# Performance work log

Hardware: AMD Instinct MI355X
Metric: run time of the kernel (lower is better)

The kernel has to match this reference:

```python
import jax, jax.numpy as jnp
import numpy as np

C = 128
K = 5
M = 150000   # num vertices
NF = 300000  # num faces
D = 192      # volume side
NEG_SLOPE = 0.2


def _x_shift(K):
    # Exactly replicates the torch module's grid construction.
    grid = np.linspace(-K // 2, K // 2, K)
    grid_3d = np.stack(np.meshgrid(grid, grid, grid), axis=0).transpose(2, 1, 3, 0)
    return jnp.asarray(grid_3d.reshape(-1, 3), jnp.float32)  # [K^3, 3]


def _trilinear_border(vol, g):
    # vol: [D1, D2, D3]; g: [N, 3] normalized coords in (x, y, z) order
    # (x -> D3/W, y -> D2/H, z -> D1/D), align_corners=True, padding_mode='border'.
    D1, D2, D3 = vol.shape
    def pix(c, S):
        return jnp.clip((c + 1.0) * 0.5 * (S - 1), 0.0, S - 1.0)
    ix, iy, iz = pix(g[:, 0], D3), pix(g[:, 1], D2), pix(g[:, 2], D1)
    x0f, y0f, z0f = jnp.floor(ix), jnp.floor(iy), jnp.floor(iz)
    wx, wy, wz = ix - x0f, iy - y0f, iz - z0f
    x0 = x0f.astype(jnp.int32); y0 = y0f.astype(jnp.int32); z0 = z0f.astype(jnp.int32)
    x1 = jnp.minimum(x0 + 1, D3 - 1)
    y1 = jnp.minimum(y0 + 1, D2 - 1)
    z1 = jnp.minimum(z0 + 1, D1 - 1)
    c000 = vol[z0, y0, x0]; c001 = vol[z0, y0, x1]
    c010 = vol[z0, y1, x0]; c011 = vol[z0, y1, x1]
    c100 = vol[z1, y0, x0]; c101 = vol[z1, y0, x1]
    c110 = vol[z1, y1, x0]; c111 = vol[z1, y1, x1]
    c00 = c000 * (1 - wx) + c001 * wx
    c01 = c010 * (1 - wx) + c011 * wx
    c10 = c100 * (1 - wx) + c101 * wx
    c11 = c110 * (1 - wx) + c111 * wx
    c0 = c00 * (1 - wy) + c01 * wy
    c1 = c10 * (1 - wy) + c11 * wy
    return c0 * (1 - wz) + c1 * wz


def _leaky(x):
    return jnp.where(x >= 0, x, NEG_SLOPE * x)


def setup_inputs() -> dict:
    key = jax.random.key(0)
    ks = jax.random.split(key, 9)
    v = jax.random.uniform(ks[0], (1, M, 3), jnp.float32, -0.9, 0.9)
    f = jax.random.randint(ks[1], (1, NF, 3), 0, M, jnp.int32)
    V = jax.random.normal(ks[2], (1, 1, D, D, D), jnp.float32)
    def init(k, shape, fan):
        return jax.random.normal(k, shape, jnp.float32) / np.sqrt(fan).astype(np.float32)
    Wconv = init(ks[3], (C, 1, K, K, K), K ** 3)
    bconv = jnp.zeros((C,), jnp.float32)
    Wlfc = init(ks[4], (C, C), C)
    blfc = jnp.zeros((C,), jnp.float32)
    W1 = init(ks[5], (C, 6), 6)
    b1 = jnp.zeros((C,), jnp.float32)
    W2 = init(ks[6], (4 * C, 2 * C), 2 * C)
    b2 = jnp.zeros((4 * C,), jnp.float32)
    W3 = init(ks[7], (2 * C, 4 * C), 4 * C)
    b3 = jnp.zeros((2 * C,), jnp.float32)
    return dict(v=v, f=f, V=V, Wconv=Wconv, bconv=bconv, Wlfc=Wlfc, blfc=blfc,
                W1=W1, b1=b1, W2=W2, b2=b2, W3=W3, b3=b3)


def reference(v, f, V, Wconv, bconv, Wlfc, blfc, W1, b1, W2, b2, W3, b3):
    m = v.shape[1]
    D1, D2, D3 = V.shape[2], V.shape[3], V.shape[4]
    Dm = max(D1, D2, D3)
    rescale = jnp.array([D3 / Dm, D2 / Dm, D1 / Dm], jnp.float32)
    x_shift = _x_shift(K)  # [K^3, 3]

    # --- cube sampling (Q = n_scale = 1), done under no_grad in torch ---
    pts = (v[0][:, None, :] + x_shift / Dm * 2.0) / rescale  # [m, K^3, 3]
    cubes = _trilinear_border(V[0, 0], pts.reshape(-1, 3)).reshape(m, K ** 3)
    cubes = jax.lax.stop_gradient(cubes)

    # --- localconv: Conv3d with full-size kernel == GEMM over flattened cube ---
    z_local = cubes @ Wconv.reshape(C, -1).T + bconv      # [m, C]
    z_local = _leaky(z_local)
    z_local = _leaky(z_local @ Wlfc.T + blfc)             # [m, C]

    # --- vertex normals (area-weighted face-normal accumulation, pytorch3d style) ---
    faces = f[0]
    vv = v[0]
    p0, p1, p2 = vv[faces[:, 0]], vv[faces[:, 1]], vv[faces[:, 2]]
    fn = jnp.cross(p1 - p0, p2 - p0)
    vn = jnp.zeros_like(vv)
    vn = vn.at[faces[:, 0]].add(fn).at[faces[:, 1]].add(fn).at[faces[:, 2]].add(fn)
    vn = vn / jnp.maximum(jnp.linalg.norm(vn, axis=-1, keepdims=True), 1e-6)

    # --- point-wise MLP fusion ---
    x = jnp.concatenate([v, vn[None]], axis=2)            # [1, m, 6]
    z_point = _leaky(x @ W1.T + b1)                       # [1, m, C]
    z = jnp.concatenate([z_point, z_local[None]], axis=2) # [1, m, 2C]
    z = _leaky(z @ W2.T + b2)                             # [1, m, 4C]
    z = _leaky(z @ W3.T + b3)                             # [1, m, 2C]
    return z
```

## Files before the change

kernel.cpp:

```cpp
#include <hip/hip_runtime.h>
#include <hip/hip_fp16.h>

#define NEG_SLOPE 0.2f

using f16x8 = __attribute__((ext_vector_type(8))) _Float16;
using f32x4 = __attribute__((ext_vector_type(4))) float;

__device__ __forceinline__ float leakyf(float x) { return x >= 0.f ? x : NEG_SLOPE * x; }

__device__ __forceinline__ void gload_lds16(const void* g, void* l) {
    __builtin_amdgcn_global_load_lds(
        (const __attribute__((address_space(1))) unsigned int*)g,
        (__attribute__((address_space(3))) unsigned int*)l, 16, 0, 0);
}

#define MFMA16(a, b, c) __builtin_amdgcn_mfma_f32_16x16x32_f16(a, b, c, 0, 0, 0)

__global__ __launch_bounds__(256)
void prelude1_kernel(const float* __restrict__ v, const int* __restrict__ f,
                     float4* __restrict__ fn4, int NF, int NE,
                     unsigned* __restrict__ gh, int fnB, int ihB, int chB,
                     int* __restrict__ codes, int* __restrict__ hist, int M,
                     const float* __restrict__ Wconv, const float* __restrict__ Wlfc,
                     const float* __restrict__ W2, const float* __restrict__ W3,
                     __half* __restrict__ wpadh, __half* __restrict__ wlfch,
                     __half* __restrict__ w2h, __half* __restrict__ w3h) {
    __shared__ unsigned h[1024];
    const int t = threadIdx.x;
    int b = blockIdx.x;
    if (b < fnB) {
        int i = b * 256 + t;
        if (i >= NF) return;
        int i0 = f[3 * i], i1 = f[3 * i + 1], i2 = f[3 * i + 2];
        float p0x = v[3 * i0], p0y = v[3 * i0 + 1], p0z = v[3 * i0 + 2];
        float ux = v[3 * i1] - p0x, uy = v[3 * i1 + 1] - p0y, uz = v[3 * i1 + 2] - p0z;
        float wx = v[3 * i2] - p0x, wy = v[3 * i2 + 1] - p0y, wz = v[3 * i2 + 2] - p0z;
        fn4[i] = make_float4(uy * wz - uz * wy, uz * wx - ux * wz, ux * wy - uy * wx, 0.f);
    } else if (b < fnB + ihB) {
        int blk = b - fnB;
        h[t] = 0; h[t + 256] = 0; h[t + 512] = 0; h[t + 768] = 0;
        __syncthreads();
        int base = blk * 4096;
#pragma unroll
        for (int k = 0; k < 16; ++k) {
            int idx = base + k * 256 + t;
            if (idx < NE) atomicAdd(&h[((unsigned)f[idx]) >> 8], 1u);
        }
        __syncthreads();
#pragma unroll
        for (int k = 0; k < 4; ++k) { int bb = t + k * 256; gh[(size_t)blk * 1024 + bb] = h[bb]; }
    } else if (b < fnB + ihB + chB) {
        int i = (b - fnB - ihB) * 256 + t;
        if (i >= M) return;
        int cx = min(max((int)((v[3 * i + 0] + 1.f) * 8.f), 0), 15);
        int cy = min(max((int)((v[3 * i + 1] + 1.f) * 8.f), 0), 15);
        int cz = min(max((int)((v[3 * i + 2] + 1.f) * 8.f), 0), 15);
        int code = 0;
#pragma unroll
        for (int bb = 0; bb < 4; ++bb)
            code |= (((cx >> bb) & 1) << (3 * bb)) | (((cy >> bb) & 1) << (3 * bb + 1)) |
                    (((cz >> bb) & 1) << (3 * bb + 2));
        codes[i] = code;
        atomicAdd(&hist[code], 1);
    } else {
        int bw = b - fnB - ihB - chB;
        if (bw < 64) {
            int i = bw * 256 + t; int ch = i >> 7, k = i & 127;
            wpadh[i] = __float2half(k < 125 ? Wconv[ch * 125 + k] : 0.f);
        } else if (bw < 128) {
            int i = (bw - 64) * 256 + t; wlfch[i] = __float2half(Wlfc[i]);
        } else if (bw < 640) {
            int i = (bw - 128) * 256 + t; w2h[i] = __float2half(W2[i]);
        } else {
            int i = (bw - 640) * 256 + t; w3h[i] = __float2half(W3[i]);
        }
    }
}

__global__ __launch_bounds__(256)
void prelude2_kernel(unsigned* __restrict__ gh, unsigned* __restrict__ binTotals, int NB,
                     const int* __restrict__ hist, int* __restrict__ offs) {
    __shared__ unsigned s[256];
    __shared__ unsigned carrySh;
    const int t = threadIdx.x;
    if (blockIdx.x < 1024) {
        const int bin = blockIdx.x;
        if (t == 0) carrySh = 0;
        __syncthreads();
        for (int base = 0; base < NB; base += 256) {
            unsigned c = carrySh;
            int i = base + t;
            unsigned val = (i < NB) ? gh[(size_t)i * 1024 + bin] : 0;
            s[t] = val;
            __syncthreads();
            for (int d = 1; d < 256; d <<= 1) {
                unsigned x = (t >= d) ? s[t - d] : 0;
                __syncthreads();
                s[t] += x;
                __syncthreads();
            }
            if (i < NB) gh[(size_t)i * 1024 + bin] = s[t] - val + c;
            if (t == 255) carrySh = c + s[255];
            __syncthreads();
        }
        if (t == 0) binTotals[bin] = carrySh;
    } else {
        if (t == 0) carrySh = 0;
        __syncthreads();
        for (int base = 0; base < 4096; base += 256) {
            unsigned c = carrySh;
            unsigned val = (unsigned)hist[base + t];
            s[t] = val;
            __syncthreads();
            for (int d = 1; d < 256; d <<= 1) {
                unsigned x = (t >= d) ? s[t - d] : 0;
                __syncthreads();
                s[t] += x;
                __syncthreads();
            }
            offs[base + t] = (int)(s[t] - val + c);
            if (t == 255) carrySh = c + s[255];
            __syncthreads();
        }
    }
}

__global__ __launch_bounds__(256)
void prelude3_kernel(const unsigned* __restrict__ binTotals, unsigned* __restrict__ binstart,
                     const int* __restrict__ codes, int* __restrict__ offs,
                     int* __restrict__ perm, int M) {
    __shared__ unsigned s[256];
    __shared__ unsigned carrySh;
    const int t = threadIdx.x;
    if (blockIdx.x == 0) {
        if (t == 0) carrySh = 0;
        __syncthreads();
        for (int base = 0; base < 1024; base += 256) {
            unsigned c = carrySh;
            unsigned val = binTotals[base + t];
            s[t] = val;
            __syncthreads();
            for (int d = 1; d < 256; d <<= 1) {
                unsigned x = (t >= d) ? s[t - d] : 0;
                __syncthreads();
                s[t] += x;
                __syncthreads();
            }
            binstart[base + t] = s[t] - val + c;
            if (t == 255) carrySh = c + s[255];
            __syncthreads();
        }
        if (t == 0) binstart[1024] = carrySh;
    } else {
        int i = (blockIdx.x - 1) * 256 + t;
        if (i >= M) return;
        int pos = atomicAdd(&offs[codes[i]], 1);
        perm[pos] = i;
    }
}

__global__ __launch_bounds__(256)
void inc_scatter_kernel(const int* __restrict__ f, const unsigned* __restrict__ gh,
                        const unsigned* __restrict__ binstart,
                        unsigned* __restrict__ sortedV, unsigned* __restrict__ sortedE,
                        int NE) {
    __shared__ unsigned loc[1024];
    const int t = threadIdx.x, blk = blockIdx.x;
#pragma unroll
    for (int k = 0; k < 4; ++k) {
        int b = t + k * 256;
        loc[b] = gh[(size_t)blk * 1024 + b] + binstart[b];
    }
    __syncthreads();
    int base = blk * 4096;
#pragma unroll
    for (int k = 0; k < 16; ++k) {
        int idx = base + k * 256 + t;
        if (idx < NE) {
            unsigned vv = (unsigned)f[idx];
            unsigned pos = atomicAdd(&loc[vv >> 8], 1u);
            sortedV[pos] = vv;
            sortedE[pos] = (unsigned)idx;
        }
    }
}

__global__ __launch_bounds__(256)
void vn_gather_kernel(const unsigned* __restrict__ sortedV, const unsigned* __restrict__ sortedE,
                      const float4* __restrict__ fn4, const unsigned* __restrict__ binstart,
                      float* __restrict__ vn, int M) {
    __shared__ float acc[768];
    const int t = threadIdx.x, b = blockIdx.x;
    acc[t] = 0.f; acc[t + 256] = 0.f; acc[t + 512] = 0.f;
    __syncthreads();
    unsigned s = binstart[b], e = binstart[b + 1];
    for (unsigned i = s + t; i < e; i += 256) {
        unsigned vv = sortedV[i];
        float4 fn = fn4[sortedE[i] / 3];
        int lv = (int)(vv & 255u) * 3;
        atomicAdd(&acc[lv + 0], fn.x);
        atomicAdd(&acc[lv + 1], fn.y);
        atomicAdd(&acc[lv + 2], fn.z);
    }
    __syncthreads();
    int gv = b * 256 + t;
    if (gv < M) {
        vn[3 * gv + 0] = acc[t * 3 + 0];
        vn[3 * gv + 1] = acc[t * 3 + 1];
        vn[3 * gv + 2] = acc[t * 3 + 2];
    }
}

__global__ __launch_bounds__(256)
void sample_kernel(const float* __restrict__ v, const float* __restrict__ vol,
                   const int* __restrict__ perm,
                   __half* __restrict__ cubes, int m_start, int cnt, int nwg, int scatter) {
    __shared__ float bbox[2][448];
    __shared__ int pi0[2][16];
    __shared__ float pw[2][16];
    const int half = threadIdx.x >> 7;
    const int q = threadIdx.x & 127;
    int q8 = nwg >> 3, r8 = nwg & 7;
    int xcd = blockIdx.x & 7, idxb = blockIdx.x >> 3;
    int bid = (xcd < r8 ? xcd * (q8 + 1) : r8 * (q8 + 1) + (xcd - r8) * q8) + idxb;
    int ml = bid * 2 + half;
    bool valid = ml < cnt;
    int m = valid ? perm[m_start + ml] : 0;

    if (valid && q < 15) {
        int axis = q / 5, idx = q - 5 * axis;
        float g = -3.f + 1.25f * (float)idx;
        float p = v[3 * m + axis] + g / 192.f * 2.f;
        float pos = fminf(fmaxf((p + 1.f) * 0.5f * 191.f, 0.f), 191.f);
        float fl = floorf(pos);
        pi0[half][q] = (int)fl;
        pw[half][q] = pos - fl;
    }
    __syncthreads();
    if (valid) {
        int xlo = pi0[half][0], ylo = pi0[half][5], zlo = pi0[half][10];
        int j = q & 63;
        int dy = j >> 3, dx = j & 7;
        if (dy < 7) {
            int X = min(xlo + dx, 191);
            int Y = min(ylo + dy, 191);
            int rowoff = dy * 9 + dx;
            const float* volYX = vol + Y * 192 + X;
#pragma unroll
            for (int k = 0; k < 4; ++k) {
                int pz = (q >> 6) + k * 2;
                if (pz < 7) {
                    int Z = min(zlo + pz, 191);
                    bbox[half][pz * 63 + rowoff] = volYX[Z * 36864];
                }
            }
        }
    }
    __syncthreads();
    if (!valid) return;
    __half* dst = cubes + (size_t)(scatter ? m : ml) * 128;
    if (q >= 125) { dst[q] = __float2half(0.f); return; }
    int a = q % 5, b = (q / 5) % 5, c = q / 25;
    int xlo = pi0[half][0], ylo = pi0[half][5], zlo = pi0[half][10];
    int gx0 = pi0[half][a], gy0 = pi0[half][5 + b], gz0 = pi0[half][10 + c];
    float wxv = pw[half][a], wyv = pw[half][5 + b], wzv = pw[half][10 + c];
    int x0 = gx0 - xlo, y0 = gy0 - ylo, z0 = gz0 - zlo;
    int x1 = min(gx0 + 1, 191) - xlo;
    int y1 = min(gy0 + 1, 191) - ylo;
    int z1 = min(gz0 + 1, 191) - zlo;
    const float* bb = bbox[half];
    int b00 = z0 * 63 + y0 * 9, b01 = z0 * 63 + y1 * 9;
    int b10 = z1 * 63 + y0 * 9, b11 = z1 * 63 + y1 * 9;
    float c000 = bb[b00 + x0], c001 = bb[b00 + x1];
    float c010 = bb[b01 + x0], c011 = bb[b01 + x1];
    float c100 = bb[b10 + x0], c101 = bb[b10 + x1];
    float c110 = bb[b11 + x0], c111 = bb[b11 + x1];
    float omx = 1.f - wxv, omy = 1.f - wyv, omz = 1.f - wzv;
    float c00 = c000 * omx + c001 * wxv;
    float c01 = c010 * omx + c011 * wxv;
    float c10 = c100 * omx + c101 * wxv;
    float c11 = c110 * omx + c111 * wxv;
    float c0 = c00 * omy + c01 * wyv;
    float c1 = c10 * omy + c11 * wyv;
    dst[25 * a + 5 * b + c] = __float2half(c0 * omz + c1 * wzv);
}

__global__ __launch_bounds__(256)
void point_kernel(const float* __restrict__ v, const float* __restrict__ vn,
                  const int* __restrict__ pvec,
                  const float* __restrict__ W1, const float* __restrict__ b1,
                  __half* __restrict__ zcat, int m_start, int cnt) {
    int ml = blockIdx.x * 2 + (threadIdx.x >> 7);
    if (ml >= cnt) return;
    int n = threadIdx.x & 127;
    int m = pvec ? pvec[m_start + ml] : (m_start + ml);
    float x0 = v[3 * m], x1 = v[3 * m + 1], x2 = v[3 * m + 2];
    float nx = vn[3 * m], ny = vn[3 * m + 1], nz = vn[3 * m + 2];
    float nrm = fmaxf(sqrtf(nx * nx + ny * ny + nz * nz), 1e-6f);
    nx /= nrm; ny /= nrm; nz /= nrm;
    const float* w = W1 + n * 6;
    float z = b1[n] + x0 * w[0] + x1 * w[1] + x2 * w[2] + nx * w[3] + ny * w[4] + nz * w[5];
    zcat[(size_t)ml * 256 + n] = __float2half(leakyf(z));
}

__global__ __launch_bounds__(256)
void convlfc_kernel(const __half* __restrict__ cubes, const __half* __restrict__ wconvh,
                    const float* __restrict__ bconv, const __half* __restrict__ wlfch,
                    const float* __restrict__ blfc, __half* __restrict__ zcat) {
    __shared__ __half Zt[128 * 128];
    __shared__ __half As[128 * 64];
    __shared__ __half Bs[128 * 64];
    const int t = threadIdx.x;
    const int lane = t & 63, wave = t >> 6;
    const int lr = lane & 15, lg = lane >> 4;
    const int wm = wave >> 1, wn = wave & 1;
    const int m0 = blockIdx.x * 128;
    const int srow = t >> 3;
    const int scb = ((t & 7) << 4) ^ (((t >> 3) & 7) << 4);
    const int swz = (lr & 7) << 4;

    const __half* Ag = cubes + (size_t)(m0 + srow) * 128 + (scb >> 1);
    const __half* Bg = wconvh + (size_t)srow * 128 + (scb >> 1);
    __half* Al = As + wave * 512;
    __half* Bl = Bs + wave * 512;
    const char* aB = (const char*)As + (wm * 64 + lr) * 128;
    const char* bB = (const char*)Bs + (wn * 64 + lr) * 128;

    f32x4 acc[4][4] = {};
    for (int kc = 0; kc < 128; kc += 64) {
#pragma unroll
        for (int i = 0; i < 4; ++i) {
            gload_lds16(Ag + (size_t)i * 32 * 128 + kc, Al + i * 2048);
            gload_lds16(Bg + (size_t)i * 32 * 128 + kc, Bl + i * 2048);
        }
        __syncthreads();
#pragma unroll
        for (int kk = 0; kk < 2; ++kk) {
            const int ko = (kk * 64 + lg * 16) ^ swz;
            f16x8 af[4], bf[4];
#pragma unroll
            for (int fx = 0; fx < 4; ++fx) {
                af[fx] = *(const f16x8*)(aB + fx * 2048 + ko);
                bf[fx] = *(const f16x8*)(bB + fx * 2048 + ko);
            }
#pragma unroll
            for (int fm = 0; fm < 4; ++fm)
#pragma unroll
                for (int fn = 0; fn < 4; ++fn)
                    acc[fm][fn] = MFMA16(af[fm], bf[fn], acc[fm][fn]);
        }
        __syncthreads();
    }
#pragma unroll
    for (int fm = 0; fm < 4; ++fm) {
#pragma unroll
        for (int fn = 0; fn < 4; ++fn) {
            int col = wn * 64 + fn * 16 + lr;
            float bias = bconv[col];
#pragma unroll
            for (int r = 0; r < 4; ++r) {
                int row = wm * 64 + fm * 16 + lg * 4 + r;
                float val = leakyf(acc[fm][fn][r] + bias);
                *(__half*)((char*)Zt + row * 256 + ((2 * col) ^ ((row & 7) << 4))) = __float2half(val);
            }
        }
    }
    __syncthreads();

    const __half* Bg2 = wlfch + (size_t)srow * 128 + (scb >> 1);
    const char* zR = (const char*)Zt + (wm * 64 + lr) * 256;
    f32x4 acc2[4][4] = {};
    for (int kc = 0; kc < 128; kc += 64) {
#pragma unroll
        for (int i = 0; i < 4; ++i)
            gload_lds16(Bg2 + (size_t)i * 32 * 128 + kc, Bl + i * 2048);
        __syncthreads();
#pragma unroll
        for (int kk = 0; kk < 2; ++kk) {
            const int kb = kc * 2 + kk * 64 + lg * 16;
            const int ko = (kk * 64 + lg * 16) ^ swz;
            f16x8 af[4], bf[4];
#pragma unroll
            for (int fx = 0; fx < 4; ++fx) {
                af[fx] = *(const f16x8*)(zR + fx * 4096 + (kb ^ swz));
                bf[fx] = *(const f16x8*)(bB + fx * 2048 + ko);
            }
#pragma unroll
            for (int fm = 0; fm < 4; ++fm)
#pragma unroll
                for (int fn = 0; fn < 4; ++fn)
                    acc2[fm][fn] = MFMA16(af[fm], bf[fn], acc2[fm][fn]);
        }
        __syncthreads();
    }
#pragma unroll
    for (int fm = 0; fm < 4; ++fm) {
#pragma unroll
        for (int fn = 0; fn < 4; ++fn) {
            int col = wn * 64 + fn * 16 + lr;
            float bias = blfc[col];
#pragma unroll
            for (int r = 0; r < 4; ++r) {
                int row = m0 + wm * 64 + fm * 16 + lg * 4 + r;
                zcat[(size_t)row * 256 + 128 + col] = __float2half(leakyf(acc2[fm][fn][r] + bias));
            }
        }
    }
}

template<bool F32OUT>
__global__ __launch_bounds__(256)
void gemm_wide(const __half* __restrict__ A, const __half* __restrict__ W,
               const float* __restrict__ bias, void* __restrict__ outp,
               int K, int Meff, int OS, int OC, const int* __restrict__ rowmap) {
    __shared__ __half As[4096];
    __shared__ __half Bs[16384];
    const int t = threadIdx.x;
    const int lane = t & 63, wave = t >> 6;
    const int lr = lane & 15, lg = lane >> 4;
    const int m0 = blockIdx.x * 64, n0 = blockIdx.y * 256;

    const int srow = t >> 3;
    const int scb = ((t & 7) << 4) ^ (((t >> 3) & 7) << 4);
    const __half* Ag = A + (size_t)(m0 + srow) * K + (scb >> 1);
    const __half* Wg = W + (size_t)(n0 + srow) * K + (scb >> 1);
    __half* Al = As + wave * 512;
    __half* Bl = Bs + wave * 512;

    const int swz = (lr & 7) << 4;
    const char* aB = (const char*)As + lr * 128;
    const char* bB = (const char*)Bs + (wave * 64 + lr) * 128;
    const int k0 = (lg * 16) ^ swz;
    const int k1 = (64 + lg * 16) ^ swz;

    f32x4 acc[4][4] = {};

    for (int kc = 0; kc < K; kc += 64) {
#pragma unroll
        for (int i = 0; i < 2; ++i)
            gload_lds16(Ag + (size_t)i * 32 * K + kc, Al + i * 2048);
#pragma unroll
        for (int i = 0; i < 8; ++i)
            gload_lds16(Wg + (size_t)i * 32 * K + kc, Bl + i * 2048);
        __syncthreads();
        f16x8 af[4], bf[4];
#pragma unroll
        for (int fx = 0; fx < 4; ++fx) {
            af[fx] = *(const f16x8*)(aB + fx * 2048 + k0);
            bf[fx] = *(const f16x8*)(bB + fx * 2048 + k0);
        }
#pragma unroll
        for (int fm = 0; fm < 4; ++fm)
#pragma unroll
            for (int fn = 0; fn < 4; ++fn)
                acc[fm][fn] = MFMA16(af[fm], bf[fn], acc[fm][fn]);
#pragma unroll
        for (int fx = 0; fx < 4; ++fx) {
            af[fx] = *(const f16x8*)(aB + fx * 2048 + k1);
            bf[fx] = *(const f16x8*)(bB + fx * 2048 + k1);
        }
#pragma unroll
        for (int fm = 0; fm < 4; ++fm)
#pragma unroll
            for (int fn = 0; fn < 4; ++fn)
                acc[fm][fn] = MFMA16(af[fm], bf[fn], acc[fm][fn]);
        __syncthreads();
    }

    float bv[4];
#pragma unroll
    for (int fn = 0; fn < 4; ++fn) bv[fn] = bias[n0 + wave * 64 + fn * 16 + lr];
    const int rbase = m0 + lg * 4;
    const int cbase = OC + n0 + wave * 64 + lr;
#pragma unroll
    for (int fm = 0; fm < 4; ++fm) {
#pragma unroll
        for (int r = 0; r < 4; ++r) {
            int row = rbase + fm * 16 + r;
            if (row < Meff) {
                size_t orow = (size_t)(rowmap ? rowmap[row] : row);
#pragma unroll
                for (int fn = 0; fn < 4; ++fn) {
                    float val = leakyf(acc[fm][fn][r] + bv[fn]);
                    if (F32OUT)
                        ((float*)outp)[orow * OS + cbase + fn * 16] = val;
                    else
                        ((__half*)outp)[orow * OS + cbase + fn * 16] = __float2half(val);
                }
            }
        }
    }
}

extern "C" void kernel_launch(void* const* d_in, const int* in_sizes, int n_in,
                              void* d_out, int out_size, void* d_ws, size_t ws_size,
                              hipStream_t stream) {
    const float* v = (const float*)d_in[0];
    const int* f = (const int*)d_in[1];
    const float* vol = (const float*)d_in[2];
    const float* Wconv = (const float*)d_in[3];
    const float* bconv = (const float*)d_in[4];
    const float* Wlfc = (const float*)d_in[5];
    const float* blfc = (const float*)d_in[6];
    const float* W1 = (const float*)d_in[7];
    const float* b1 = (const float*)d_in[8];
    const float* W2 = (const float*)d_in[9];
    const float* b2 = (const float*)d_in[10];
    const float* W3 = (const float*)d_in[11];
    const float* b3 = (const float*)d_in[12];
    float* out = (float*)d_out;
    const int M = in_sizes[0] / 3;
    const int NF = in_sizes[1] / 3;
    const int NE = 3 * NF;
    const int NB = (NE + 4095) / 4096;

    char* base = (char*)d_ws;
    float* vn = (float*)base;
    size_t off = ((size_t)M * 12 + 255) & ~(size_t)255;
    int* codes = (int*)(base + off); off += ((size_t)M * 4 + 255) & ~(size_t)255;
    int* perm  = (int*)(base + off); off += ((size_t)M * 4 + 255) & ~(size_t)255;
    int* hist  = (int*)(base + off); off += 4096 * 4;
    int* offs  = (int*)(base + off); off += 4096 * 4;
    float4* fn4 = (float4*)(base + off); off += (size_t)NF * 16;
    unsigned* sortedV = (unsigned*)(base + off); off += ((size_t)NE * 4 + 255) & ~(size_t)255;
    unsigned* sortedE = (unsigned*)(base + off); off += ((size_t)NE * 4 + 255) & ~(size_t)255;
    unsigned* gh = (unsigned*)(base + off); off += ((size_t)1024 * NB * 4 + 255) & ~(size_t)255;
    unsigned* binstart = (unsigned*)(base + off); off += 1032 * 4;
    unsigned* binTotals = (unsigned*)(base + off); off += 1024 * 4;
    __half* wpadh = (__half*)(base + off); off += 32768;
    __half* wlfch = (__half*)(base + off); off += 32768;
    __half* w2h = (__half*)(base + off); off += 262144;
    __half* w3h = (__half*)(base + off); off += 262144;
    size_t avail = ws_size > off ? ws_size - off : 0;
    size_t Mpad = ((size_t)M + 127) & ~(size_t)127;
    size_t chm = (avail / 1792) & ~(size_t)127;
    if (chm > Mpad) chm = Mpad;
    if (chm < 128) chm = 128;
    const bool single = (chm >= (size_t)M);
    __half* cubes = (__half*)(base + off);
    __half* zcat = cubes + chm * 128;
    __half* h = zcat + chm * 256;

    const int fnB = (NF + 255) / 256;
    const int chB = (M + 255) / 256;

    hipMemsetAsync(hist, 0, 4096 * 4, stream);
    prelude1_kernel<<<fnB + NB + chB + 1152, 256, 0, stream>>>(
        v, f, fn4, NF, NE, gh, fnB, NB, chB, codes, hist, M,
        Wconv, Wlfc, W2, W3, wpadh, wlfch, w2h, w3h);
    prelude2_kernel<<<1025, 256, 0, stream>>>(gh, binTotals, NB, hist, offs);
    prelude3_kernel<<<1 + chB, 256, 0, stream>>>(binTotals, binstart, codes, offs, perm, M);
    inc_scatter_kernel<<<NB, 256, 0, stream>>>(f, gh, binstart, sortedV, sortedE, NE);
    vn_gather_kernel<<<(M + 255) / 256, 256, 0, stream>>>(sortedV, sortedE, fn4, binstart, vn, M);

    for (size_t ms = 0; ms < (size_t)M; ms += chm) {
        size_t rem = (size_t)M - ms;
        int cnt = (int)(rem < chm ? rem : chm);
        int mb = (cnt + 127) / 128;
        int mb64 = (cnt + 63) / 64;
        int nblk = (cnt + 1) / 2;
        sample_kernel<<<nblk, 256, 0, stream>>>(v, vol, perm, cubes, (int)ms, cnt, nblk,
                                                single ? 1 : 0);
        convlfc_kernel<<<mb, 256, 0, stream>>>(cubes, wpadh, bconv, wlfch, blfc, zcat);
        point_kernel<<<(cnt + 1) / 2, 256, 0, stream>>>(
            v, vn, single ? nullptr : perm, W1, b1, zcat, (int)ms, cnt);
        gemm_wide<false><<<dim3(mb64, 2), 256, 0, stream>>>(
            zcat, w2h, b2, h, 256, mb64 * 64, 512, 0, nullptr);
        gemm_wide<true><<<dim3(mb64, 1), 256, 0, stream>>>(
            h, w3h, b3, out, 512, cnt, 256, 0, single ? nullptr : (perm + ms));
    }
}
```

Baseline: 477.9 us.

## Double-buffer LDS tiles in gemm_wide to overlap global loads with MFMA

Splits the A and B shared-memory tiles in gemm_wide into two buffers and prefetches the next two K-chunks with direct global-to-LDS loads. Manual vmcnt waits and raw barriers let the loads for chunk k+2 run while chunk k is being computed. The aim is to hide global memory latency behind the MFMA work. This doubles LDS use to about 80KB per block, which may reduce occupancy, and the vmcnt(10) count must match exactly the ten loads issued per chunk.

```diff
diff --git a/kernel.cpp b/kernel.cpp
--- a/kernel.cpp
+++ b/kernel.cpp
@@ -413,8 +413,8 @@
 void gemm_wide(const __half* __restrict__ A, const __half* __restrict__ W,
                const float* __restrict__ bias, void* __restrict__ outp,
                int K, int Meff, int OS, int OC, const int* __restrict__ rowmap) {
-    __shared__ __half As[4096];
-    __shared__ __half Bs[16384];
+    __shared__ __half As[2][4096];
+    __shared__ __half Bs[2][16384];
     const int t = threadIdx.x;
     const int lane = t & 63, wave = t >> 6;
     const int lr = lane & 15, lg = lane >> 4;
@@ -424,47 +424,73 @@
     const int scb = ((t & 7) << 4) ^ (((t >> 3) & 7) << 4);
     const __half* Ag = A + (size_t)(m0 + srow) * K + (scb >> 1);
     const __half* Wg = W + (size_t)(n0 + srow) * K + (scb >> 1);
-    __half* Al = As + wave * 512;
-    __half* Bl = Bs + wave * 512;
 
     const int swz = (lr & 7) << 4;
-    const char* aB = (const char*)As + lr * 128;
-    const char* bB = (const char*)Bs + (wave * 64 + lr) * 128;
+    const int aOff = lr * 128;
+    const int bOff = (wave * 64 + lr) * 128;
     const int k0 = (lg * 16) ^ swz;
     const int k1 = (64 + lg * 16) ^ swz;
 
     f32x4 acc[4][4] = {};
 
+#pragma unroll
+    for (int bufi = 0; bufi < 2; ++bufi) {
+        __half* Al = As[bufi] + wave * 512;
+        __half* Bl = Bs[bufi] + wave * 512;
+#pragma unroll
+        for (int i = 0; i < 2; ++i)
+            gload_lds16(Ag + (size_t)i * 32 * K + bufi * 64, Al + i * 2048);
+#pragma unroll
+        for (int i = 0; i < 8; ++i)
+            gload_lds16(Wg + (size_t)i * 32 * K + bufi * 64, Bl + i * 2048);
+    }
+
+    int cur = 0;
     for (int kc = 0; kc < K; kc += 64) {
-#pragma unroll
-        for (int i = 0; i < 2; ++i)
-            gload_lds16(Ag + (size_t)i * 32 * K + kc, Al + i * 2048);
-#pragma unroll
-        for (int i = 0; i < 8; ++i)
-            gload_lds16(Wg + (size_t)i * 32 * K + kc, Bl + i * 2048);
-        __syncthreads();
-        f16x8 af[4], bf[4];
-#pragma unroll
-        for (int fx = 0; fx < 4; ++fx) {
-            af[fx] = *(const f16x8*)(aB + fx * 2048 + k0);
-            bf[fx] = *(const f16x8*)(bB + fx * 2048 + k0);
-        }
-#pragma unroll
-        for (int fm = 0; fm < 4; ++fm)
-#pragma unroll
-            for (int fn = 0; fn < 4; ++fn)
-                acc[fm][fn] = MFMA16(af[fm], bf[fn], acc[fm][fn]);
-#pragma unroll
-        for (int fx = 0; fx < 4; ++fx) {
-            af[fx] = *(const f16x8*)(aB + fx * 2048 + k1);
-            bf[fx] = *(const f16x8*)(bB + fx * 2048 + k1);
-        }
-#pragma unroll
-        for (int fm = 0; fm < 4; ++fm)
-#pragma unroll
-            for (int fn = 0; fn < 4; ++fn)
-                acc[fm][fn] = MFMA16(af[fm], bf[fn], acc[fm][fn]);
-        __syncthreads();
+        if (kc + 64 < K)
+            asm volatile("s_waitcnt vmcnt(10)" ::: "memory");
+        else
+            asm volatile("s_waitcnt vmcnt(0)" ::: "memory");
+        __builtin_amdgcn_s_barrier();
+        __builtin_amdgcn_sched_barrier(0);
+        {
+            const char* aB = (const char*)As[cur] + aOff;
+            const char* bB = (const char*)Bs[cur] + bOff;
+            f16x8 af[4], bf[4];
+#pragma unroll
+            for (int fx = 0; fx < 4; ++fx) {
+                af[fx] = *(const f16x8*)(aB + fx * 2048 + k0);
+                bf[fx] = *(const f16x8*)(bB + fx * 2048 + k0);
+            }
+#pragma unroll
+            for (int fm = 0; fm < 4; ++fm)
+#pragma unroll
+                for (int fn = 0; fn < 4; ++fn)
+                    acc[fm][fn] = MFMA16(af[fm], bf[fn], acc[fm][fn]);
+#pragma unroll
+            for (int fx = 0; fx < 4; ++fx) {
+                af[fx] = *(const f16x8*)(aB + fx * 2048 + k1);
+                bf[fx] = *(const f16x8*)(bB + fx * 2048 + k1);
+            }
+#pragma unroll
+            for (int fm = 0; fm < 4; ++fm)
+#pragma unroll
+                for (int fn = 0; fn < 4; ++fn)
+                    acc[fm][fn] = MFMA16(af[fm], bf[fn], acc[fm][fn]);
+        }
+        __builtin_amdgcn_sched_barrier(0);
+        __builtin_amdgcn_s_barrier();
+        if (kc + 128 < K) {
+            __half* Al = As[cur] + wave * 512;
+            __half* Bl = Bs[cur] + wave * 512;
+#pragma unroll
+            for (int i = 0; i < 2; ++i)
+                gload_lds16(Ag + (size_t)i * 32 * K + kc + 128, Al + i * 2048);
+#pragma unroll
+            for (int i = 0; i < 8; ++i)
+                gload_lds16(Wg + (size_t)i * 32 * K + kc + 128, Bl + i * 2048);
+        }
+        cur ^= 1;
     }
 
     float bv[4];
```

Result: slower. 496.5 us (+3.9%).
